# Optimization experiments

Measured on AMD Instinct MI355X. Metric: run time of the kernel, lower is better.

Reference implementation:

```python
import jax, jax.numpy as jnp
import numpy as np

V, D, L, H, SLOTS, FF = 32000, 1024, 6, 16, 4096, 4096
DH = D // H

def rmsnorm(x, w, eps=1e-8):
    return x * jax.lax.rsqrt(jnp.mean(x * x, axis=-1, keepdims=True) + eps) * w

def rope(x):
    # x: [B,T,D]; interleaved RoPE over full d_model as in RoPEEmbedding
    T = x.shape[1]
    inv_freq = 1.0 / (10000.0 ** (jnp.arange(0, D, 2, dtype=jnp.float32) / D))
    freqs = jnp.arange(T, dtype=jnp.float32)[:, None] * inv_freq[None, :]  # [T, D/2]
    cos, sin = jnp.cos(freqs), jnp.sin(freqs)
    x1, x2 = x[..., ::2], x[..., 1::2]
    out = jnp.stack([x1 * cos - x2 * sin, x1 * sin + x2 * cos], axis=-1)
    return out.reshape(x.shape)

def block(x, Wq, Wk, Wv, Wo, bo, n1, Wg, Wu, Wd, n2):
    B, T, _ = x.shape
    q = (x @ Wq).reshape(B, T, H, DH)
    k = (x @ Wk).reshape(B, T, H, DH)
    v = (x @ Wv).reshape(B, T, H, DH)
    scores = jnp.einsum('bqhd,bkhd->bhqk', q, k) * (DH ** -0.5)
    attn = jax.nn.softmax(scores, axis=-1)
    o = jnp.einsum('bhqk,bkhd->bqhd', attn, v).reshape(B, T, D)
    x = rmsnorm(x + o @ Wo + bo, n1)
    ff = (jax.nn.silu(x @ Wg) * (x @ Wu)) @ Wd
    return rmsnorm(x + ff, n2)

def setup_inputs() -> dict:
    key = jax.random.key(0)
    ks = jax.random.split(key, 20)
    nrm = lambda k, s: (jax.random.normal(k, s, jnp.float32) * 0.02)
    inp = {
        'ids': jax.random.randint(ks[0], (2, 2048), 0, V),
        'tok_embed': nrm(ks[1], (V, D)),
        'Wq': nrm(ks[2], (L, D, D)), 'Wk': nrm(ks[3], (L, D, D)),
        'Wv': nrm(ks[4], (L, D, D)), 'Wo': nrm(ks[5], (L, D, D)),
        'bo': jnp.zeros((L, D), jnp.float32),
        'n1': jnp.ones((L, D), jnp.float32),
        'Wg': nrm(ks[6], (L, D, FF)), 'Wu': nrm(ks[7], (L, D, FF)),
        'Wd': nrm(ks[8], (L, FF, D)),
        'n2': jnp.ones((L, D), jnp.float32),
        'mem': nrm(ks[9], (SLOTS, D)),
        'Wsp': nrm(ks[10], (D, D)), 'bsp': jnp.zeros((D,), jnp.float32),
        'Wrp': nrm(ks[11], (D, D)), 'brp': jnp.zeros((D,), jnp.float32),
        'nout': jnp.ones((D,), jnp.float32),
    }
    return inp

def reference(ids, tok_embed, Wq, Wk, Wv, Wo, bo, n1, Wg, Wu, Wd, n2,
              mem, Wsp, bsp, Wrp, brp, nout):
    x = tok_embed[ids]            # [B,T,D] gather
    x = rope(x)
    for i in range(L):
        x = block(x, Wq[i], Wk[i], Wv[i], Wo[i], bo[i], n1[i],
                  Wg[i], Wu[i], Wd[i], n2[i])
    # StateBank content-addressed read: route queries over memory slots
    q = x @ Wsp + bsp                                   # [B,T,D]
    slot_scores = jnp.einsum('btd,sd->bts', q, mem) * (D ** -0.5)
    attention_maps = jax.nn.softmax(slot_scores, axis=-1)  # [B,T,SLOTS]
    r = jnp.einsum('bts,sd->btd', attention_maps, mem)     # gather-route read
    r = r @ Wrp + brp
    h = rmsnorm(x + r, nout)
    logits = h @ tok_embed.T      # tied lm_head
    return logits
```

## Files before the change

### kernel.cpp

```cpp
#include <hip/hip_runtime.h>

typedef __bf16 bf16;
typedef __attribute__((ext_vector_type(8))) __bf16 bf16x8;
typedef __attribute__((ext_vector_type(4))) __bf16 bf16x4;
typedef __attribute__((ext_vector_type(4))) float f32x4;

#define NL 6
#define DIM 1024
#define NH 16
#define DH 64
#define TT 2048
#define BB 2
#define BT 4096
#define FFD 4096
#define NSLOT 4096
#define NV 32000

__device__ __forceinline__ void gld16(const void* g, void* l) {
  __builtin_amdgcn_global_load_lds(
      (const __attribute__((address_space(1))) void*)g,
      (__attribute__((address_space(3))) void*)l, 16, 0, 0);
}


__global__ void cvt_bf16(const float* __restrict__ s, bf16* __restrict__ d, long n) {
  long i = ((long)blockIdx.x * 256 + threadIdx.x) * 4;
  if (i + 3 < n) {
    float4 v = *(const float4*)(s + i);
    bf16x4 o = {(bf16)v.x, (bf16)v.y, (bf16)v.z, (bf16)v.w};
    *(bf16x4*)(d + i) = o;
  }
}

__global__ void transpose_cvt(const float* __restrict__ src, bf16* __restrict__ dst, int R, int C) {
  __shared__ float tile[32][33];
  int c0 = blockIdx.x * 32, r0 = blockIdx.y * 32;
  int tx = threadIdx.x;
  int ty = threadIdx.y;
  float4 v = *(const float4*)(src + (size_t)(r0 + ty) * C + c0 + tx * 4);
  tile[ty][tx * 4 + 0] = v.x;
  tile[ty][tx * 4 + 1] = v.y;
  tile[ty][tx * 4 + 2] = v.z;
  tile[ty][tx * 4 + 3] = v.w;
  __syncthreads();
  bf16x4 o = {(bf16)tile[tx * 4 + 0][ty], (bf16)tile[tx * 4 + 1][ty],
              (bf16)tile[tx * 4 + 2][ty], (bf16)tile[tx * 4 + 3][ty]};
  *(bf16x4*)(dst + (size_t)(c0 + ty) * R + r0 + tx * 4) = o;
}

__global__ void transpose_v(const bf16* __restrict__ v, int ldv, bf16* __restrict__ vT) {
  __shared__ bf16 tile[32][33];
  int t0 = blockIdx.x * 32, d0 = blockIdx.y * 32, bh = blockIdx.z;
  int b = bh >> 4, h = bh & 15;
  int tx = threadIdx.x, ty = threadIdx.y;
#pragma unroll
  for (int i = 0; i < 4; ++i)
    tile[ty + i * 8][tx] = v[(size_t)(b * TT + t0 + ty + i * 8) * ldv + h * DH + d0 + tx];
  __syncthreads();
#pragma unroll
  for (int i = 0; i < 4; ++i)
    vT[((size_t)bh * DH + d0 + ty + i * 8) * TT + t0 + tx] = tile[tx][ty + i * 8];
}


__global__ void embed_rope(const int* __restrict__ ids, const float* __restrict__ emb,
                           float* __restrict__ xf, bf16* __restrict__ xb) {
  int bt = blockIdx.x;
  int t = bt & (TT - 1);
  int id = ids[bt];
  const float* row = emb + (size_t)id * DIM;
  for (int p = threadIdx.x; p < DIM / 2; p += 256) {
    float x1 = row[2 * p], x2 = row[2 * p + 1];
    float inv = __expf(-9.210340371976184f * (float)p * (1.0f / 512.0f));
    float ang = (float)t * inv;
    float c = cosf(ang), s = sinf(ang);
    float o1 = x1 * c - x2 * s;
    float o2 = x1 * s + x2 * c;
    size_t base = (size_t)bt * DIM + 2 * p;
    xf[base] = o1; xf[base + 1] = o2;
    xb[base] = (bf16)o1; xb[base + 1] = (bf16)o2;
  }
}

enum { EP_BF16 = 0, EP_F32 = 1, EP_F32_BIAS = 2, EP_BF16_BIAS = 3, EP_SILU_MUL = 4 };


template <int EP>
__global__ __launch_bounds__(512, 1) void gemm8(
    const bf16* __restrict__ A, const bf16* __restrict__ Bt, void* __restrict__ Cp,
    const float* __restrict__ bias, const bf16* __restrict__ aux,
    int M, int N, int K) {
  __shared__ bf16 S[4][2][256 * 32];

  const int tid = threadIdx.x;
  const int lane = tid & 63;
  const int r16 = lane & 15, hi = lane >> 4;
  const int wave = tid >> 6;
  const int wm = wave >> 2, wn = wave & 3;

  const int nwg = gridDim.x;
  const int orig = blockIdx.x;
  const int qq = nwg >> 3, rr = nwg & 7;
  const int xcd = orig & 7, cidx = orig >> 3;
  const int wg = (xcd < rr ? xcd * (qq + 1) : rr * (qq + 1) + (xcd - rr) * qq) + cidx;
  const int gM = M / 256;
  const int m0 = (wg % gM) * 256;
  const int n0 = (wg / gM) * 256;

  const int srow = tid >> 2;
  const int ccol = tid & 3;
  const int skey = (srow >> 1) & 3;
  const int gcol = (ccol ^ skey) * 8;
  const bf16* aS = A + (size_t)(m0 + srow) * K + gcol;
  const bf16* bS = Bt + (size_t)(n0 + srow) * K + gcol;
  const int dst0 = tid * 8;

  const int rkey = (r16 >> 1) & 3;
  const int rchunk = (hi ^ rkey) * 8;

  f32x4 acc[8][4] = {};
  const int NT = K / 32;

#pragma unroll
  for (int s = 0; s < 3; ++s) {
    gld16(aS + s * 32, &S[s][0][dst0]);
    gld16(aS + s * 32 + (size_t)128 * K, &S[s][0][dst0 + 4096]);
    gld16(bS + s * 32, &S[s][1][dst0]);
    gld16(bS + s * 32 + (size_t)128 * K, &S[s][1][dst0 + 4096]);
  }
  asm volatile("s_waitcnt vmcnt(8)" ::: "memory");
  __builtin_amdgcn_s_barrier();
  __builtin_amdgcn_sched_barrier(0);

  for (int s = 0; s < NT; ++s) {
    const int cs = s & 3, ps = (s + 3) & 3;
    const bool pre = (s + 3) < NT;
    const bf16* SA = S[cs][0];
    const bf16* SB = S[cs][1];
    const size_t koff = (size_t)(s + 3) * 32;
    bf16x8 af[4], bfr[4];

#pragma unroll
    for (int j = 0; j < 4; ++j)
      bfr[j] = *(const bf16x8*)&SB[(wn * 64 + j * 16 + r16) * 32 + rchunk];
#pragma unroll
    for (int i = 0; i < 4; ++i)
      af[i] = *(const bf16x8*)&SA[(wm * 128 + i * 16 + r16) * 32 + rchunk];
    if (pre) {
      gld16(aS + koff, &S[ps][0][dst0]);
      gld16(aS + koff + (size_t)128 * K, &S[ps][0][dst0 + 4096]);
    }
    __builtin_amdgcn_s_barrier();
    __builtin_amdgcn_sched_barrier(0);
    __builtin_amdgcn_s_setprio(1);
#pragma unroll
    for (int i = 0; i < 4; ++i)
#pragma unroll
      for (int j = 0; j < 4; ++j)
        acc[i][j] = __builtin_amdgcn_mfma_f32_16x16x32_bf16(af[i], bfr[j], acc[i][j], 0, 0, 0);
    __builtin_amdgcn_s_setprio(0);
    __builtin_amdgcn_s_barrier();
    __builtin_amdgcn_sched_barrier(0);

#pragma unroll
    for (int i = 0; i < 4; ++i)
      af[i] = *(const bf16x8*)&SA[(wm * 128 + 64 + i * 16 + r16) * 32 + rchunk];
    if (pre) {
      gld16(bS + koff, &S[ps][1][dst0]);
      gld16(bS + koff + (size_t)128 * K, &S[ps][1][dst0 + 4096]);
    }
    __builtin_amdgcn_s_barrier();
    __builtin_amdgcn_sched_barrier(0);
    __builtin_amdgcn_s_setprio(1);
#pragma unroll
    for (int i = 0; i < 4; ++i)
#pragma unroll
      for (int j = 0; j < 4; ++j)
        acc[4 + i][j] = __builtin_amdgcn_mfma_f32_16x16x32_bf16(af[i], bfr[j], acc[4 + i][j], 0, 0, 0);
    __builtin_amdgcn_s_setprio(0);
    if (pre)               asm volatile("s_waitcnt vmcnt(8)" ::: "memory");
    else if ((s + 2) < NT) asm volatile("s_waitcnt vmcnt(4)" ::: "memory");
    else if ((s + 1) < NT) asm volatile("s_waitcnt vmcnt(0)" ::: "memory");
    __builtin_amdgcn_s_barrier();
    __builtin_amdgcn_sched_barrier(0);
  }

#pragma unroll
  for (int mi = 0; mi < 8; ++mi) {
    const int m = m0 + wm * 128 + mi * 16 + hi * 4;
#pragma unroll
    for (int j = 0; j < 4; ++j) {
      const int n = n0 + wn * 64 + j * 16 + r16;
#pragma unroll
      for (int q = 0; q < 4; ++q) {
        size_t idx = (size_t)(m + q) * N + n;
        float v = acc[mi][j][q];
        if constexpr (EP == EP_F32) {
          ((float*)Cp)[idx] = v;
        } else if constexpr (EP == EP_F32_BIAS) {
          ((float*)Cp)[idx] = v + bias[n];
        } else if constexpr (EP == EP_BF16) {
          ((bf16*)Cp)[idx] = (bf16)v;
        } else if constexpr (EP == EP_BF16_BIAS) {
          ((bf16*)Cp)[idx] = (bf16)(v + bias[n]);
        } else {
          float sg = v / (1.0f + __expf(-v));
          ((bf16*)Cp)[idx] = (bf16)(sg * (float)aux[idx]);
        }
      }
    }
  }
}


template <int BM, int BN, int WMW, int WNW, int EP>
__global__ __launch_bounds__(WMW * WNW * 64, 2) void gemmk(
    const bf16* __restrict__ A, const bf16* __restrict__ Bt, void* __restrict__ Cp,
    const float* __restrict__ bias, const bf16* __restrict__ aux,
    int M, int N, int K) {
  constexpr int BK = 32;
  constexpr int MF = BM / (WMW * 16);
  constexpr int NF = BN / (WNW * 16);
  constexpr int LA = BM / 64;
  constexpr int LB = BN / 64;
  constexpr int VM_MAIN = 2 * LA + LB;
  constexpr int VM_TAIL = LA + LB;
  __shared__ bf16 sA[4][BM * BK];
  __shared__ bf16 sB[4][BN * BK];

  const int tid = threadIdx.x;
  const int lane = tid & 63;
  const int r16 = lane & 15, hi = lane >> 4;
  const int wave = tid >> 6;
  const int wm = wave / WNW, wn = wave % WNW;

  const int nwg = gridDim.x;
  const int orig = blockIdx.x;
  const int qq = nwg >> 3, rr = nwg & 7;
  const int xcd = orig & 7, cidx = orig >> 3;
  const int wg = (xcd < rr ? xcd * (qq + 1) : rr * (qq + 1) + (xcd - rr) * qq) + cidx;
  const int gM = M / BM;
  const int m0 = (wg % gM) * BM;
  const int n0 = (wg / gM) * BN;

  const int srow = tid >> 2;
  const int ccol = tid & 3;
  const int skey = (srow >> 1) & 3;
  const int gcol = ((ccol ^ skey)) * 8;
  const bf16* aS = A + (size_t)(m0 + srow) * K + gcol;
  const bf16* bS = Bt + (size_t)(n0 + srow) * K + gcol;
  const int dst0 = srow * BK + ccol * 8;

  const int rkey = (r16 >> 1) & 3;
  const int rchunk = (hi ^ rkey) * 8;

  f32x4 acc[MF][NF] = {};
  const int NT = K / BK;

#pragma unroll
  for (int t0_ = 0; t0_ < 2; ++t0_) {
#pragma unroll
    for (int p = 0; p < LA; ++p)
      gld16(aS + t0_ * BK + (size_t)p * 64 * K, &sA[t0_][dst0 + p * 64 * BK]);
#pragma unroll
    for (int p = 0; p < LB; ++p)
      gld16(bS + t0_ * BK + (size_t)p * 64 * K, &sB[t0_][dst0 + p * 64 * BK]);
  }

  for (int t = 0; t < NT; ++t) {
    const int cb = t & 3;
    const int pb = (t + 2) & 3;
    const bool pre = (t + 2) < NT;
    if (pre) {
#pragma unroll
      for (int p = 0; p < LA; ++p)
        gld16(aS + (size_t)(t + 2) * BK + (size_t)p * 64 * K, &sA[pb][dst0 + p * 64 * BK]);
    }
    if (pre)             asm volatile("s_waitcnt vmcnt(%0)" :: "i"(VM_MAIN) : "memory");
    else if (t + 1 < NT) asm volatile("s_waitcnt vmcnt(%0)" :: "i"(VM_TAIL) : "memory");
    else                 asm volatile("s_waitcnt vmcnt(0)" ::: "memory");
    __builtin_amdgcn_s_barrier();
    __builtin_amdgcn_sched_barrier(0);

    bf16x8 bf_[NF];
#pragma unroll
    for (int j = 0; j < NF; ++j)
      bf_[j] = *(const bf16x8*)&sB[cb][(wn * (NF * 16) + j * 16 + r16) * BK + rchunk];
    if (pre) {
#pragma unroll
      for (int p = 0; p < LB; ++p)
        gld16(bS + (size_t)(t + 2) * BK + (size_t)p * 64 * K, &sB[pb][dst0 + p * 64 * BK]);
    }
    bf16x8 af[MF];
#pragma unroll
    for (int i = 0; i < MF; ++i)
      af[i] = *(const bf16x8*)&sA[cb][(wm * (MF * 16) + i * 16 + r16) * BK + rchunk];
    __builtin_amdgcn_s_setprio(1);
#pragma unroll
    for (int i = 0; i < MF; ++i)
#pragma unroll
      for (int j = 0; j < NF; ++j)
        acc[i][j] = __builtin_amdgcn_mfma_f32_16x16x32_bf16(af[i], bf_[j], acc[i][j], 0, 0, 0);
    __builtin_amdgcn_s_setprio(0);
  }

#pragma unroll
  for (int i = 0; i < MF; ++i) {
    const int m = m0 + wm * (MF * 16) + i * 16 + hi * 4;
#pragma unroll
    for (int j = 0; j < NF; ++j) {
      const int n = n0 + wn * (NF * 16) + j * 16 + r16;
#pragma unroll
      for (int q = 0; q < 4; ++q) {
        size_t idx = (size_t)(m + q) * N + n;
        float v = acc[i][j][q];
        if constexpr (EP == EP_F32) {
          ((float*)Cp)[idx] = v;
        } else if constexpr (EP == EP_F32_BIAS) {
          ((float*)Cp)[idx] = v + bias[n];
        } else if constexpr (EP == EP_BF16) {
          ((bf16*)Cp)[idx] = (bf16)v;
        } else if constexpr (EP == EP_BF16_BIAS) {
          ((bf16*)Cp)[idx] = (bf16)(v + bias[n]);
        } else {
          float sg = v / (1.0f + __expf(-v));
          ((bf16*)Cp)[idx] = (bf16)(sg * (float)aux[idx]);
        }
      }
    }
  }
}


__global__ __launch_bounds__(256, 2) void attn_flash(
    const bf16* __restrict__ Qp, const bf16* __restrict__ Kp, int ldk,
    const bf16* __restrict__ Vt, bf16* __restrict__ Op) {
  __shared__ bf16 Ks[2][128 * 32];
  __shared__ bf16 Vs[4][64 * 32];
  __shared__ bf16 Ps[4][2][16 * 144];
  const int tid = threadIdx.x, lane = tid & 63, wave = tid >> 6;
  const int h = blockIdx.y, b = blockIdx.z;
  const int r16 = lane & 15, hi = lane >> 4;
  const int qbase = blockIdx.x * 128 + wave * 32;

  const float QS = 0.1803368801f;
  bf16x8 qa[2][2];
#pragma unroll
  for (int f = 0; f < 2; ++f) {
    const bf16* qp = Qp + (size_t)(b * TT + qbase + f * 16 + r16) * ldk + h * DH + hi * 8;
    bf16x8 q0 = *(const bf16x8*)qp;
    bf16x8 q1 = *(const bf16x8*)(qp + 32);
#pragma unroll
    for (int e = 0; e < 8; ++e) {
      qa[f][0][e] = (bf16)((float)q0[e] * QS);
      qa[f][1][e] = (bf16)((float)q1[e] * QS);
    }
  }
  const bf16* kBase = Kp + (size_t)(b * TT) * ldk + h * DH;
  const bf16* vBase = Vt + (size_t)(b * NH + h) * DH * TT;

  const int srow = tid >> 2, ccol = tid & 3;
  const int skey = (srow >> 1) & 3;
  const int scolS = (ccol ^ skey) * 8;
  const int dstc = ccol * 8;
  const int rkey = (r16 >> 1) & 3;
  const int rchunk = (hi ^ rkey) * 8;

  float m_run[2] = {-1e30f, -1e30f};
  float l_run[2] = {0.f, 0.f};
  f32x4 oacc[2][4] = {};

  for (int kt = 0; kt < TT; kt += 128) {
#pragma unroll
    for (int half = 0; half < 2; ++half) {
      gld16(kBase + (size_t)(kt + srow) * ldk + half * 32 + scolS, &Ks[half][srow * 32 + dstc]);
      gld16(kBase + (size_t)(kt + 64 + srow) * ldk + half * 32 + scolS, &Ks[half][(64 + srow) * 32 + dstc]);
    }
#pragma unroll
    for (int ks = 0; ks < 4; ++ks)
      gld16(vBase + (size_t)srow * TT + kt + ks * 32 + scolS, &Vs[ks][srow * 32 + dstc]);
    __syncthreads();

#pragma unroll
    for (int f = 0; f < 2; ++f) {
      f32x4 s[8];
      __builtin_amdgcn_s_setprio(1);
#pragma unroll
      for (int kg = 0; kg < 8; ++kg) {
        f32x4 z = {};
        bf16x8 kb0 = *(const bf16x8*)&Ks[0][(kg * 16 + r16) * 32 + rchunk];
        bf16x8 kb1 = *(const bf16x8*)&Ks[1][(kg * 16 + r16) * 32 + rchunk];
        z = __builtin_amdgcn_mfma_f32_16x16x32_bf16(kb0, qa[f][0], z, 0, 0, 0);
        z = __builtin_amdgcn_mfma_f32_16x16x32_bf16(kb1, qa[f][1], z, 0, 0, 0);
        s[kg] = z;
      }
      __builtin_amdgcn_s_setprio(0);

      float pm = s[0][0];
#pragma unroll
      for (int kg = 0; kg < 8; ++kg)
#pragma unroll
        for (int i = 0; i < 4; ++i) pm = fmaxf(pm, s[kg][i]);
      pm = fmaxf(pm, __shfl_xor(pm, 16));
      pm = fmaxf(pm, __shfl_xor(pm, 32));

      if (!__all(pm - m_run[f] <= 11.5411f)) {
        float mnew = fmaxf(m_run[f], pm);
        float fr = exp2f(m_run[f] - mnew);
        m_run[f] = mnew;
        l_run[f] *= fr;
#pragma unroll
        for (int i = 0; i < 4; ++i) {
          float fi = __shfl(fr, hi * 4 + i);
#pragma unroll
          for (int n = 0; n < 4; ++n) oacc[f][n][i] *= fi;
        }
      }

      float lsum = 0.f;
#pragma unroll
      for (int kg = 0; kg < 8; ++kg) {
        float p0 = exp2f(s[kg][0] - m_run[f]);
        float p1 = exp2f(s[kg][1] - m_run[f]);
        float p2 = exp2f(s[kg][2] - m_run[f]);
        float p3 = exp2f(s[kg][3] - m_run[f]);
        lsum += (p0 + p1) + (p2 + p3);
        bf16x4 pk = {(bf16)p0, (bf16)p1, (bf16)p2, (bf16)p3};
        *(bf16x4*)&Ps[wave][f][r16 * 144 + kg * 16 + hi * 4] = pk;
      }
      l_run[f] += lsum;

      __builtin_amdgcn_s_setprio(1);
#pragma unroll
      for (int ks = 0; ks < 4; ++ks) {
        bf16x8 pa = *(const bf16x8*)&Ps[wave][f][r16 * 144 + ks * 32 + hi * 8];
#pragma unroll
        for (int n = 0; n < 4; ++n) {
          bf16x8 vb = *(const bf16x8*)&Vs[ks][(n * 16 + r16) * 32 + rchunk];
          oacc[f][n] = __builtin_amdgcn_mfma_f32_16x16x32_bf16(pa, vb, oacc[f][n], 0, 0, 0);
        }
      }
      __builtin_amdgcn_s_setprio(0);
    }
    __syncthreads();
  }

#pragma unroll
  for (int f = 0; f < 2; ++f) {
    float lq = l_run[f];
    lq += __shfl_xor(lq, 16);
    lq += __shfl_xor(lq, 32);
    float invq = 1.0f / lq;
#pragma unroll
    for (int i = 0; i < 4; ++i) {
      float inv_i = __shfl(invq, hi * 4 + i);
      int trow = qbase + f * 16 + hi * 4 + i;
      size_t base = ((size_t)b * TT + trow) * DIM + h * DH;
#pragma unroll
      for (int n = 0; n < 4; ++n)
        Op[base + n * 16 + r16] = (bf16)(oacc[f][n][i] * inv_i);
    }
  }
}


__global__ __launch_bounds__(256) void resid_rms(
    const float* __restrict__ xin, const float* __restrict__ y, const float* __restrict__ wgt,
    float* __restrict__ xf_out, bf16* __restrict__ xb_out) {
  __shared__ float red[4];
  const int r = blockIdx.x, tid = threadIdx.x;
  const size_t base = (size_t)r * DIM + tid * 4;
  float4 v = *(const float4*)(xin + base);
  float4 u = *(const float4*)(y + base);
  v.x += u.x; v.y += u.y; v.z += u.z; v.w += u.w;
  float ss = v.x * v.x + v.y * v.y + v.z * v.z + v.w * v.w;
#pragma unroll
  for (int d = 1; d < 64; d <<= 1) ss += __shfl_xor(ss, d);
  if ((tid & 63) == 0) red[tid >> 6] = ss;
  __syncthreads();
  ss = red[0] + red[1] + red[2] + red[3];
  float sc = rsqrtf(ss * (1.0f / DIM) + 1e-8f);
  const float4 wv = *(const float4*)(wgt + tid * 4);
  float o0 = v.x * sc * wv.x, o1 = v.y * sc * wv.y, o2 = v.z * sc * wv.z, o3 = v.w * sc * wv.w;
  if (xf_out) {
    float4 ov = {o0, o1, o2, o3};
    *(float4*)(xf_out + base) = ov;
  }
  bf16x4 ob = {(bf16)o0, (bf16)o1, (bf16)o2, (bf16)o3};
  *(bf16x4*)(xb_out + base) = ob;
}


__global__ __launch_bounds__(256) void softmax_rows(const float* __restrict__ Sc, bf16* __restrict__ P) {
  __shared__ float red[4];
  const int r = blockIdx.x, tid = threadIdx.x;
  const float* row = Sc + (size_t)r * NSLOT;
  float4 v[4];
#pragma unroll
  for (int i = 0; i < 4; ++i) v[i] = *(const float4*)(row + tid * 4 + i * 1024);
  float mx = -1e30f;
#pragma unroll
  for (int i = 0; i < 4; ++i)
    mx = fmaxf(fmaxf(fmaxf(fmaxf(mx, v[i].x), v[i].y), v[i].z), v[i].w);
#pragma unroll
  for (int d = 1; d < 64; d <<= 1) mx = fmaxf(mx, __shfl_xor(mx, d));
  if ((tid & 63) == 0) red[tid >> 6] = mx;
  __syncthreads();
  mx = fmaxf(fmaxf(red[0], red[1]), fmaxf(red[2], red[3]));
  __syncthreads();
  float e[16];
  float sum = 0.f;
#pragma unroll
  for (int i = 0; i < 4; ++i) {
    e[i * 4 + 0] = __expf((v[i].x - mx) * 0.03125f);
    e[i * 4 + 1] = __expf((v[i].y - mx) * 0.03125f);
    e[i * 4 + 2] = __expf((v[i].z - mx) * 0.03125f);
    e[i * 4 + 3] = __expf((v[i].w - mx) * 0.03125f);
    sum += e[i * 4 + 0] + e[i * 4 + 1] + e[i * 4 + 2] + e[i * 4 + 3];
  }
#pragma unroll
  for (int d = 1; d < 64; d <<= 1) sum += __shfl_xor(sum, d);
  if ((tid & 63) == 0) red[tid >> 6] = sum;
  __syncthreads();
  sum = red[0] + red[1] + red[2] + red[3];
  float inv = 1.0f / sum;
#pragma unroll
  for (int i = 0; i < 4; ++i) {
    bf16x4 ob = {(bf16)(e[i * 4 + 0] * inv), (bf16)(e[i * 4 + 1] * inv),
                 (bf16)(e[i * 4 + 2] * inv), (bf16)(e[i * 4 + 3] * inv)};
    *(bf16x4*)(P + (size_t)r * NSLOT + tid * 4 + i * 1024) = ob;
  }
}


extern "C" void kernel_launch(void* const* d_in, const int* in_sizes, int n_in,
                              void* d_out, int out_size, void* d_ws, size_t ws_size,
                              hipStream_t stream) {
  (void)in_sizes; (void)n_in; (void)out_size;
  const int* ids = (const int*)d_in[0];
  const float* emb = (const float*)d_in[1];
  const float* Wq = (const float*)d_in[2];
  const float* Wk = (const float*)d_in[3];
  const float* Wv = (const float*)d_in[4];
  const float* Wo = (const float*)d_in[5];
  const float* bo = (const float*)d_in[6];
  const float* n1 = (const float*)d_in[7];
  const float* Wg = (const float*)d_in[8];
  const float* Wu = (const float*)d_in[9];
  const float* Wd = (const float*)d_in[10];
  const float* n2 = (const float*)d_in[11];
  const float* memp = (const float*)d_in[12];
  const float* Wsp = (const float*)d_in[13];
  const float* bsp = (const float*)d_in[14];
  const float* Wrp = (const float*)d_in[15];
  const float* brp = (const float*)d_in[16];
  const float* nout = (const float*)d_in[17];

  char* w = (char*)d_ws;
  auto alloc = [&](size_t bytes) -> void* {
    void* p = (void*)w;
    w += (bytes + 255) & ~(size_t)255;
    return p;
  };

  const size_t dd = (size_t)DIM * DIM;
  const size_t dff = (size_t)DIM * FFD;

  bf16* tok_b = (bf16*)alloc((size_t)NV * DIM * 2);
  bf16* mem_b = (bf16*)alloc((size_t)NSLOT * DIM * 2);
  bf16* memT  = (bf16*)alloc((size_t)NSLOT * DIM * 2);
  bf16* WspT  = (bf16*)alloc(dd * 2);
  bf16* WrpT  = (bf16*)alloc(dd * 2);
  float* xf   = (float*)alloc((size_t)BT * DIM * 4);
  bf16* xb    = (bf16*)alloc((size_t)BT * DIM * 2);
  float* yb   = (float*)alloc((size_t)BT * DIM * 4);
  bf16* W3T   = (bf16*)alloc(3 * dd * 2);
  bf16* WoT   = (bf16*)alloc(dd * 2);
  bf16* WgT   = (bf16*)alloc(dff * 2);
  bf16* WuT   = (bf16*)alloc(dff * 2);
  bf16* WdT   = (bf16*)alloc(dff * 2);
  bf16* qkv   = (bf16*)alloc((size_t)BT * 3 * DIM * 2);
  bf16* vT_   = (bf16*)alloc((size_t)BT * DIM * 2);
  bf16* ot_   = (bf16*)alloc((size_t)BT * DIM * 2);
  bf16* qb    = (bf16*)alloc((size_t)BT * DIM * 2);
  bf16* rb    = (bf16*)alloc((size_t)BT * DIM * 2);
  bf16* hb    = (bf16*)alloc((size_t)BT * DIM * 2);

  size_t used = (size_t)(w - (char*)d_ws);
  size_t region_bytes = (size_t)BT * NSLOT * 4 + (size_t)BT * NSLOT * 2;
  char* region;
  if (used + region_bytes <= ws_size) region = (char*)alloc(region_bytes);
  else region = (char*)d_out;
  bf16* Ub = (bf16*)region;
  bf16* Hb = (bf16*)(region + (size_t)BT * FFD * 2);
  float* scoresF = (float*)region;
  bf16* attnb = (bf16*)(region + (size_t)BT * NSLOT * 4);

  dim3 blkT(8, 32);
  dim3 blkV(32, 8);

  cvt_bf16<<<NV * DIM / 1024, 256, 0, stream>>>(emb, tok_b, (long)NV * DIM);
  cvt_bf16<<<NSLOT * DIM / 1024, 256, 0, stream>>>(memp, mem_b, (long)NSLOT * DIM);
  transpose_cvt<<<dim3(DIM / 32, NSLOT / 32), blkT, 0, stream>>>(memp, memT, NSLOT, DIM);
  transpose_cvt<<<dim3(DIM / 32, DIM / 32), blkT, 0, stream>>>(Wsp, WspT, DIM, DIM);
  transpose_cvt<<<dim3(DIM / 32, DIM / 32), blkT, 0, stream>>>(Wrp, WrpT, DIM, DIM);
  embed_rope<<<BT, 256, 0, stream>>>(ids, emb, xf, xb);

  for (int l = 0; l < NL; ++l) {
    transpose_cvt<<<dim3(32, 32), blkT, 0, stream>>>(Wq + l * dd, W3T, DIM, DIM);
    transpose_cvt<<<dim3(32, 32), blkT, 0, stream>>>(Wk + l * dd, W3T + dd, DIM, DIM);
    transpose_cvt<<<dim3(32, 32), blkT, 0, stream>>>(Wv + l * dd, W3T + 2 * dd, DIM, DIM);
    transpose_cvt<<<dim3(32, 32), blkT, 0, stream>>>(Wo + l * dd, WoT, DIM, DIM);
    transpose_cvt<<<dim3(FFD / 32, DIM / 32), blkT, 0, stream>>>(Wg + l * dff, WgT, DIM, FFD);
    transpose_cvt<<<dim3(FFD / 32, DIM / 32), blkT, 0, stream>>>(Wu + l * dff, WuT, DIM, FFD);
    transpose_cvt<<<dim3(DIM / 32, FFD / 32), blkT, 0, stream>>>(Wd + l * dff, WdT, FFD, DIM);

    gemm8<EP_BF16><<<dim3(16 * 12), 512, 0, stream>>>(
        xb, W3T, qkv, nullptr, nullptr, BT, 3 * DIM, DIM);
    transpose_v<<<dim3(TT / 32, DH / 32, BB * NH), blkV, 0, stream>>>(qkv + 2 * DIM, 3 * DIM, vT_);
    attn_flash<<<dim3(TT / 128, NH, BB), 256, 0, stream>>>(qkv, qkv + DIM, 3 * DIM, vT_, ot_);
    gemmk<128, 64, 2, 2, EP_F32_BIAS><<<dim3(32 * 16), 256, 0, stream>>>(
        ot_, WoT, yb, bo + l * DIM, nullptr, BT, DIM, DIM);
    resid_rms<<<BT, 256, 0, stream>>>(xf, yb, n1 + l * DIM, xf, xb);
    gemm8<EP_BF16><<<dim3(16 * 16), 512, 0, stream>>>(
        xb, WuT, Ub, nullptr, nullptr, BT, FFD, DIM);
    gemm8<EP_SILU_MUL><<<dim3(16 * 16), 512, 0, stream>>>(
        xb, WgT, Hb, nullptr, Ub, BT, FFD, DIM);
    gemmk<128, 64, 2, 2, EP_F32><<<dim3(32 * 16), 256, 0, stream>>>(
        Hb, WdT, yb, nullptr, nullptr, BT, DIM, FFD);
    resid_rms<<<BT, 256, 0, stream>>>(xf, yb, n2 + l * DIM, xf, xb);
  }

  gemmk<128, 64, 2, 2, EP_BF16_BIAS><<<dim3(32 * 16), 256, 0, stream>>>(
      xb, WspT, qb, bsp, nullptr, BT, DIM, DIM);
  gemm8<EP_F32><<<dim3(16 * 16), 512, 0, stream>>>(
      qb, mem_b, scoresF, nullptr, nullptr, BT, NSLOT, DIM);
  softmax_rows<<<BT, 256, 0, stream>>>(scoresF, attnb);
  gemmk<128, 64, 2, 2, EP_BF16><<<dim3(32 * 16), 256, 0, stream>>>(
      attnb, memT, rb, nullptr, nullptr, BT, DIM, NSLOT);
  gemmk<128, 64, 2, 2, EP_F32_BIAS><<<dim3(32 * 16), 256, 0, stream>>>(
      rb, WrpT, yb, brp, nullptr, BT, DIM, DIM);
  resid_rms<<<BT, 256, 0, stream>>>(xf, yb, nout, nullptr, hb);
  gemm8<EP_F32><<<dim3(16 * 125), 512, 0, stream>>>(
      hb, tok_b, (float*)d_out, nullptr, nullptr, BT, NV, DIM);
}
```

Measured before the change: 2.759 ms.

## Fuse gate and up FFN GEMMs into one dual-B kernel; nontemporal logits store

Adds a gemm8ff kernel that loads one A tile and both the up and gate weight tiles. It accumulates both products and applies SiLU(g)*u in the epilogue, so the bf16 U intermediate is no longer written and read back, and A is staged once instead of twice. Tiles are 256x128 with two accumulator sets, which raises register pressure and launches twice as many workgroups. Separately, the final logits GEMM now uses nontemporal stores to avoid polluting the cache with the large output.

```diff
diff --git a/kernel.cpp b/kernel.cpp
--- a/kernel.cpp
+++ b/kernel.cpp
@@ -82,7 +82,7 @@
   }
 }
 
-enum { EP_BF16 = 0, EP_F32 = 1, EP_F32_BIAS = 2, EP_BF16_BIAS = 3, EP_SILU_MUL = 4 };
+enum { EP_BF16 = 0, EP_F32 = 1, EP_F32_BIAS = 2, EP_BF16_BIAS = 3, EP_SILU_MUL = 4, EP_F32_NT = 5 };
 
 
 template <int EP>
@@ -197,6 +197,8 @@
         float v = acc[mi][j][q];
         if constexpr (EP == EP_F32) {
           ((float*)Cp)[idx] = v;
+        } else if constexpr (EP == EP_F32_NT) {
+          __builtin_nontemporal_store(v, &((float*)Cp)[idx]);
         } else if constexpr (EP == EP_F32_BIAS) {
           ((float*)Cp)[idx] = v + bias[n];
         } else if constexpr (EP == EP_BF16) {
@@ -207,6 +209,129 @@
           float sg = v / (1.0f + __expf(-v));
           ((bf16*)Cp)[idx] = (bf16)(sg * (float)aux[idx]);
         }
+      }
+    }
+  }
+}
+
+
+__global__ __launch_bounds__(512, 1) void gemm8ff(
+    const bf16* __restrict__ A, const bf16* __restrict__ Bu, const bf16* __restrict__ Bg,
+    bf16* __restrict__ Cp, int M, int N, int K) {
+  __shared__ bf16 SA[4][256 * 32];
+  __shared__ bf16 SU[4][128 * 32];
+  __shared__ bf16 SG[4][128 * 32];
+
+  const int tid = threadIdx.x;
+  const int lane = tid & 63;
+  const int r16 = lane & 15, hi = lane >> 4;
+  const int wave = tid >> 6;
+  const int wm = wave >> 2, wn = wave & 3;
+
+  const int nwg = gridDim.x;
+  const int orig = blockIdx.x;
+  const int qq = nwg >> 3, rr = nwg & 7;
+  const int xcd = orig & 7, cidx = orig >> 3;
+  const int wg = (xcd < rr ? xcd * (qq + 1) : rr * (qq + 1) + (xcd - rr) * qq) + cidx;
+  const int gM = M / 256;
+  const int m0 = (wg % gM) * 256;
+  const int n0 = (wg / gM) * 128;
+
+  const int srow = tid >> 2;
+  const int ccol = tid & 3;
+  const int skey = (srow >> 1) & 3;
+  const int gcol = (ccol ^ skey) * 8;
+  const bf16* aS = A + (size_t)(m0 + srow) * K + gcol;
+  const bf16* uS = Bu + (size_t)(n0 + srow) * K + gcol;
+  const bf16* gSp = Bg + (size_t)(n0 + srow) * K + gcol;
+  const int dst0 = tid * 8;
+
+  const int rkey = (r16 >> 1) & 3;
+  const int rchunk = (hi ^ rkey) * 8;
+
+  f32x4 accU[8][2] = {}, accG[8][2] = {};
+  const int NT = K / 32;
+
+#pragma unroll
+  for (int s = 0; s < 3; ++s) {
+    gld16(aS + s * 32, &SA[s][dst0]);
+    gld16(aS + s * 32 + (size_t)128 * K, &SA[s][dst0 + 4096]);
+    gld16(uS + s * 32, &SU[s][dst0]);
+    gld16(gSp + s * 32, &SG[s][dst0]);
+  }
+  asm volatile("s_waitcnt vmcnt(8)" ::: "memory");
+  __builtin_amdgcn_s_barrier();
+  __builtin_amdgcn_sched_barrier(0);
+
+  for (int s = 0; s < NT; ++s) {
+    const int cs = s & 3, ps = (s + 3) & 3;
+    const bool pre = (s + 3) < NT;
+    const size_t koff = (size_t)(s + 3) * 32;
+    bf16x8 af[4], bu[2], bg[2];
+
+#pragma unroll
+    for (int j = 0; j < 2; ++j) {
+      bu[j] = *(const bf16x8*)&SU[cs][(wn * 32 + j * 16 + r16) * 32 + rchunk];
+      bg[j] = *(const bf16x8*)&SG[cs][(wn * 32 + j * 16 + r16) * 32 + rchunk];
+    }
+#pragma unroll
+    for (int i = 0; i < 4; ++i)
+      af[i] = *(const bf16x8*)&SA[cs][(wm * 128 + i * 16 + r16) * 32 + rchunk];
+    if (pre) {
+      gld16(aS + koff, &SA[ps][dst0]);
+      gld16(aS + koff + (size_t)128 * K, &SA[ps][dst0 + 4096]);
+    }
+    __builtin_amdgcn_s_barrier();
+    __builtin_amdgcn_sched_barrier(0);
+    __builtin_amdgcn_s_setprio(1);
+#pragma unroll
+    for (int i = 0; i < 4; ++i)
+#pragma unroll
+      for (int j = 0; j < 2; ++j) {
+        accU[i][j] = __builtin_amdgcn_mfma_f32_16x16x32_bf16(af[i], bu[j], accU[i][j], 0, 0, 0);
+        accG[i][j] = __builtin_amdgcn_mfma_f32_16x16x32_bf16(af[i], bg[j], accG[i][j], 0, 0, 0);
+      }
+    __builtin_amdgcn_s_setprio(0);
+    __builtin_amdgcn_s_barrier();
+    __builtin_amdgcn_sched_barrier(0);
+
+#pragma unroll
+    for (int i = 0; i < 4; ++i)
+      af[i] = *(const bf16x8*)&SA[cs][(wm * 128 + 64 + i * 16 + r16) * 32 + rchunk];
+    if (pre) {
+      gld16(uS + koff, &SU[ps][dst0]);
+      gld16(gSp + koff, &SG[ps][dst0]);
+    }
+    __builtin_amdgcn_s_barrier();
+    __builtin_amdgcn_sched_barrier(0);
+    __builtin_amdgcn_s_setprio(1);
+#pragma unroll
+    for (int i = 0; i < 4; ++i)
+#pragma unroll
+      for (int j = 0; j < 2; ++j) {
+        accU[4 + i][j] = __builtin_amdgcn_mfma_f32_16x16x32_bf16(af[i], bu[j], accU[4 + i][j], 0, 0, 0);
+        accG[4 + i][j] = __builtin_amdgcn_mfma_f32_16x16x32_bf16(af[i], bg[j], accG[4 + i][j], 0, 0, 0);
+      }
+    __builtin_amdgcn_s_setprio(0);
+    if (pre)               asm volatile("s_waitcnt vmcnt(8)" ::: "memory");
+    else if ((s + 2) < NT) asm volatile("s_waitcnt vmcnt(4)" ::: "memory");
+    else if ((s + 1) < NT) asm volatile("s_waitcnt vmcnt(0)" ::: "memory");
+    __builtin_amdgcn_s_barrier();
+    __builtin_amdgcn_sched_barrier(0);
+  }
+
+#pragma unroll
+  for (int mi = 0; mi < 8; ++mi) {
+    const int m = m0 + wm * 128 + mi * 16 + hi * 4;
+#pragma unroll
+    for (int j = 0; j < 2; ++j) {
+      const int n = n0 + wn * 32 + j * 16 + r16;
+#pragma unroll
+      for (int q = 0; q < 4; ++q) {
+        float u = accU[mi][j][q];
+        float g = accG[mi][j][q];
+        float sg = g / (1.0f + __expf(-g));
+        Cp[(size_t)(m + q) * N + n] = (bf16)(sg * u);
       }
     }
   }
@@ -591,8 +716,7 @@
   char* region;
   if (used + region_bytes <= ws_size) region = (char*)alloc(region_bytes);
   else region = (char*)d_out;
-  bf16* Ub = (bf16*)region;
-  bf16* Hb = (bf16*)(region + (size_t)BT * FFD * 2);
+  bf16* Hb = (bf16*)region;
   float* scoresF = (float*)region;
   bf16* attnb = (bf16*)(region + (size_t)BT * NSLOT * 4);
 
@@ -622,10 +746,8 @@
     gemmk<128, 64, 2, 2, EP_F32_BIAS><<<dim3(32 * 16), 256, 0, stream>>>(
         ot_, WoT, yb, bo + l * DIM, nullptr, BT, DIM, DIM);
     resid_rms<<<BT, 256, 0, stream>>>(xf, yb, n1 + l * DIM, xf, xb);
-    gemm8<EP_BF16><<<dim3(16 * 16), 512, 0, stream>>>(
-        xb, WuT, Ub, nullptr, nullptr, BT, FFD, DIM);
-    gemm8<EP_SILU_MUL><<<dim3(16 * 16), 512, 0, stream>>>(
-        xb, WgT, Hb, nullptr, Ub, BT, FFD, DIM);
+    gemm8ff<<<dim3(16 * 32), 512, 0, stream>>>(
+        xb, WuT, WgT, Hb, BT, FFD, DIM);
     gemmk<128, 64, 2, 2, EP_F32><<<dim3(32 * 16), 256, 0, stream>>>(
         Hb, WdT, yb, nullptr, nullptr, BT, DIM, FFD);
     resid_rms<<<BT, 256, 0, stream>>>(xf, yb, n2 + l * DIM, xf, xb);
@@ -641,6 +763,6 @@
   gemmk<128, 64, 2, 2, EP_F32_BIAS><<<dim3(32 * 16), 256, 0, stream>>>(
       rb, WrpT, yb, brp, nullptr, BT, DIM, DIM);
   resid_rms<<<BT, 256, 0, stream>>>(xf, yb, nout, nullptr, hb);
-  gemm8<EP_F32><<<dim3(16 * 125), 512, 0, stream>>>(
+  gemm8<EP_F32_NT><<<dim3(16 * 125), 512, 0, stream>>>(
       hb, tok_b, (float*)d_out, nullptr, nullptr, BT, NV, DIM);
 }
```

Result: no change. 2.711 ms (-1.7%).
